# Optimization experiments

Hardware: AMD Instinct MI355X
Metric: run time of the kernel (lower is better)

## Reference

```python
import jax, jax.numpy as jnp
import numpy as np

N, E, G = 50000, 800000, 64
IN, HID, H, OUT = 128, 64, 4, 10


def _gat_layer(x, src, dst, W, a_src, a_dst, b):
    # x: [N, Fin]; W: [H*C, Fin]; a_src/a_dst: [H, C]; b: [H*C]
    n = x.shape[0]
    C = a_src.shape[1]
    h = (x @ W.T).reshape(n, H, C)                      # [N, H, C]
    e_src = jnp.einsum('nhc,hc->nh', h, a_src)          # [N, H]
    e_dst = jnp.einsum('nhc,hc->nh', h, a_dst)          # [N, H]
    logits = jax.nn.leaky_relu(e_src[src] + e_dst[dst], 0.2)  # [E', H]
    # segment softmax over destination node
    m = jax.ops.segment_max(logits, dst, num_segments=n)
    ex = jnp.exp(logits - m[dst])
    denom = jax.ops.segment_sum(ex, dst, num_segments=n)
    alpha = ex / (denom[dst] + 1e-16)                   # [E', H]
    msg = h[src] * alpha[:, :, None]                    # [E', H, C]
    out = jax.ops.segment_sum(msg, dst, num_segments=n) # [N, H, C]
    return out.reshape(n, H * C) + b


def setup_inputs() -> dict:
    key = jax.random.key(0)
    ks = jax.random.split(key, 20)
    x = jax.random.normal(ks[0], (N, IN), dtype=jnp.float32)
    edge_index = jax.random.randint(ks[1], (2, E), 0, N, dtype=jnp.int64)
    batch = jnp.sort(jax.random.randint(ks[2], (N,), 0, G, dtype=jnp.int64))

    def glorot(k, shape):
        fan = shape[-1]
        return jax.random.normal(k, shape, dtype=jnp.float32) / jnp.sqrt(jnp.float32(fan))

    ins = [IN, HID * H, HID * H]
    params = {}
    for i, fin in enumerate(ins, start=1):
        params[f'W{i}'] = glorot(ks[3 * i], (H * HID, fin))
        params[f'a_src{i}'] = glorot(ks[3 * i + 1], (H, HID))
        params[f'a_dst{i}'] = glorot(ks[3 * i + 2], (H, HID))
        params[f'b{i}'] = jnp.zeros((H * HID,), dtype=jnp.float32)
    params['Wl'] = glorot(ks[13], (OUT, H * HID))
    params['bl'] = jnp.zeros((OUT,), dtype=jnp.float32)
    return dict(x=x, edge_index=edge_index, batch=batch, **params)


def reference(x, edge_index, batch,
              W1, a_src1, a_dst1, b1,
              W2, a_src2, a_dst2, b2,
              W3, a_src3, a_dst3, b3,
              Wl, bl):
    n = x.shape[0]
    loops = jnp.arange(n, dtype=edge_index.dtype)
    src = jnp.concatenate([edge_index[0], loops])  # add self-loops (PyG default)
    dst = jnp.concatenate([edge_index[1], loops])

    h = jax.nn.elu(_gat_layer(x, src, dst, W1, a_src1, a_dst1, b1))
    h = jax.nn.elu(_gat_layer(h, src, dst, W2, a_src2, a_dst2, b2))
    h = _gat_layer(h, src, dst, W3, a_src3, a_dst3, b3)

    # global mean pool over graphs
    sums = jax.ops.segment_sum(h, batch, num_segments=G)          # [G, H*HID]
    counts = jax.ops.segment_sum(jnp.ones((n,), h.dtype), batch, num_segments=G)
    pooled = sums / jnp.maximum(counts, 1.0)[:, None]
    return pooled @ Wl.T + bl                                      # [G, OUT]
```

## Files before the change

kernel.cpp:

```cpp
#include <hip/hip_runtime.h>
#include <hip/hip_bf16.h>
#include <math.h>

#define NNODES 50000
#define NEDGES 800000
#define NGRAPH 64
#define FIN 128
#define HC 256
#define NHEAD 4
#define NOUT 10
#define ETOT (NEDGES + NNODES)
#define NB196 ((NNODES + 255) / 256)


typedef unsigned short u16;
typedef unsigned char u8;
typedef __attribute__((ext_vector_type(8))) short short8;
typedef __attribute__((ext_vector_type(4))) float f32x4;
typedef __attribute__((ext_vector_type(2))) float f32x2;

__device__ inline u16 f2b(float f) {
    union { float f; unsigned u; } v; v.f = f;
    unsigned r = v.u + 0x7FFF + ((v.u >> 16) & 1);
    return (u16)(r >> 16);
}
__device__ inline float b2f(u16 u) {
    union { unsigned u; float f; } v; v.u = ((unsigned)u) << 16; return v.f;
}

__device__ inline void gload_lds16(const void* g, void* l) {
    __builtin_amdgcn_global_load_lds(
        (const __attribute__((address_space(1))) unsigned*)g,
        (__attribute__((address_space(3))) unsigned*)l, 16, 0, 0);
}


#define CS0 (NNODES * FIN)
#define CS1 (HC * FIN)
#define CS2 (HC * HC)
#define NBCONV (((CS0 + CS1 + 2 * CS2) / 4 + 255) / 256)
#define NBDEG ((ETOT + 255) / 256)

__global__ void prep_kernel(const float* __restrict__ x, const float* __restrict__ W1,
                            const float* __restrict__ W2, const float* __restrict__ W3,
                            u16* __restrict__ xb, u16* __restrict__ w1b,
                            u16* __restrict__ w2b, u16* __restrict__ w3b,
                            const int* __restrict__ ei, int* __restrict__ deg) {
    int b = blockIdx.x;
    if (b < NBCONV) {
        long i = (long)(b * 256 + threadIdx.x) * 4;
        if (i < CS0) {
            float4 v = *(const float4*)(x + i);
            ushort4 o;
            o.x = f2b(v.x); o.y = f2b(v.y); o.z = f2b(v.z); o.w = f2b(v.w);
            *(ushort4*)(xb + i) = o;
        } else if (i < CS0 + CS1) {
            long off = i - CS0;
            float4 v = *(const float4*)(W1 + off);
            ushort4 o;
            o.x = f2b(v.x); o.y = f2b(v.y); o.z = f2b(v.z); o.w = f2b(v.w);
            *(ushort4*)(w1b + off) = o;
        } else if (i < CS0 + CS1 + 2 * CS2) {
            const float* src; u16* dst; long off;
            if (i < CS0 + CS1 + CS2) { src = W2; dst = w2b; off = i - CS0 - CS1; }
            else                     { src = W3; dst = w3b; off = i - CS0 - CS1 - CS2; }
            float4 v = *(const float4*)(src + off);
            int row = (int)(off >> 8), col = (int)(off & 255);
            float vv[4] = {v.x, v.y, v.z, v.w};
            #pragma unroll
            for (int k = 0; k < 4; ++k) {
                int c = col + k;
                int pp = (c & ~63) | ((c & 15) << 2) | ((c >> 4) & 3);
                dst[row * 256 + pp] = f2b(vv[k]);
            }
        }
    } else {
        int e = (b - NBCONV) * 256 + threadIdx.x;
        if (e >= ETOT) return;
        int dstn = (e < NEDGES) ? ei[NEDGES + e] : (e - NEDGES);
        atomicAdd(&deg[dstn], 1);
    }
}


__global__ __launch_bounds__(256) void scan1_kernel(const int* __restrict__ deg,
                                                    int* __restrict__ off,
                                                    int* __restrict__ bsum) {
    int tid = threadIdx.x, lane = tid & 63, wid = tid >> 6;
    int i = blockIdx.x * 256 + tid;
    __shared__ int ws[4];
    int v = (i < NNODES) ? deg[i] : 0;
    int x = v;
    #pragma unroll
    for (int o = 1; o < 64; o <<= 1) {
        int t = __shfl_up(x, o);
        if (lane >= o) x += t;
    }
    if (lane == 63) ws[wid] = x;
    __syncthreads();
    if (tid < 4) {
        int w = ws[tid];
        #pragma unroll
        for (int o = 1; o < 4; o <<= 1) {
            int t = __shfl_up(w, o, 4);
            if ((tid & 3) >= o) w += t;
        }
        ws[tid] = w;
    }
    __syncthreads();
    int wexcl = wid ? ws[wid - 1] : 0;
    if (i <= NNODES) off[i] = x - v + wexcl;
    if (tid == 0) bsum[blockIdx.x] = ws[3];
}

__global__ __launch_bounds__(256) void scan2_kernel(int* __restrict__ bsum,
                                                    const int* __restrict__ batch,
                                                    int* __restrict__ goff) {
    int tid = threadIdx.x, lane = tid & 63, wid = tid >> 6;
    __shared__ int ws[4];
    int v = (tid < NB196) ? bsum[tid] : 0;
    int x = v;
    #pragma unroll
    for (int o = 1; o < 64; o <<= 1) {
        int t = __shfl_up(x, o);
        if (lane >= o) x += t;
    }
    if (lane == 63) ws[wid] = x;
    __syncthreads();
    if (tid < 4) {
        int w = ws[tid];
        #pragma unroll
        for (int o = 1; o < 4; o <<= 1) {
            int t = __shfl_up(w, o, 4);
            if ((tid & 3) >= o) w += t;
        }
        ws[tid] = w;
    }
    __syncthreads();
    int wexcl = wid ? ws[wid - 1] : 0;
    if (tid < NB196) bsum[tid] = x - v + wexcl;
    if (tid <= NGRAPH) {
        int g = tid, lo = 0, hi = NNODES;
        while (lo < hi) {
            int mid = (lo + hi) >> 1;
            if (batch[mid] < g) lo = mid + 1; else hi = mid;
        }
        goff[g] = lo;
    }
}

__global__ void scatter_kernel(const int* __restrict__ ei, const int* __restrict__ off,
                               const int* __restrict__ bsum,
                               int* __restrict__ cur, int* __restrict__ ssrc) {
    int e = blockIdx.x * blockDim.x + threadIdx.x;
    if (e >= ETOT) return;
    int src, dst;
    if (e < NEDGES) { src = ei[e]; dst = ei[NEDGES + e]; }
    else            { src = dst = e - NEDGES; }
    int pos = off[dst] + bsum[dst >> 8] + atomicAdd(&cur[dst], 1);
    ssrc[pos] = src;
}


#define TBM 128
#define TBN 128
#define TBK 32

__global__ __launch_bounds__(256) void gemm_mfma(const u16* __restrict__ A,
                                                 const u16* __restrict__ B,
                                                 u8* __restrict__ C, int K,
                                                 const float* __restrict__ asrc,
                                                 const float* __restrict__ adst,
                                                 float* __restrict__ es,
                                                 float* __restrict__ ed) {
    __shared__ u16 Als[TBM * TBK];
    __shared__ u16 Bls[TBN * TBK];
    int tid = threadIdx.x;
    int wave = tid >> 6, lane = tid & 63;
    int brow = blockIdx.x * TBM, bcol = blockIdx.y * TBN;
    int m_base = (wave >> 1) * 64, n_base = (wave & 1) * 64;
    int r0 = tid >> 2, kc = (tid & 3) * 8;
    int lquad = lane >> 4, l16 = lane & 15;

    f32x4 acc[4][4] = {};

    const u16* ga0 = A + (size_t)(brow + r0) * K + kc;
    const u16* ga1 = A + (size_t)(brow + 64 + r0) * K + kc;
    const u16* gb0 = B + (size_t)(bcol + r0) * K + kc;
    const u16* gb1 = B + (size_t)(bcol + 64 + r0) * K + kc;
    u16* la0 = &Als[r0 * TBK + kc];
    u16* la1 = &Als[(64 + r0) * TBK + kc];
    u16* lb0 = &Bls[r0 * TBK + kc];
    u16* lb1 = &Bls[(64 + r0) * TBK + kc];

    for (int k0 = 0; k0 < K; k0 += TBK) {
        __syncthreads();
        gload_lds16(ga0 + k0, la0);
        gload_lds16(ga1 + k0, la1);
        gload_lds16(gb0 + k0, lb0);
        gload_lds16(gb1 + k0, lb1);
        __syncthreads();
        short8 fa[4], fb[4];
        #pragma unroll
        for (int i = 0; i < 4; ++i) {
            fa[i] = *(const short8*)(&Als[(m_base + i * 16 + l16) * TBK + lquad * 8]);
            fb[i] = *(const short8*)(&Bls[(n_base + i * 16 + l16) * TBK + lquad * 8]);
        }
        #pragma unroll
        for (int i = 0; i < 4; ++i)
            #pragma unroll
            for (int j = 0; j < 4; ++j)
                acc[i][j] = __builtin_amdgcn_mfma_f32_16x16x32_bf16(fa[i], fb[j], acc[i][j], 0, 0, 0);
    }

    #pragma unroll
    for (int i = 0; i < 4; ++i) {
        int rbase = brow + m_base + i * 16 + lquad * 4;
        #pragma unroll
        for (int r = 0; r < 4; ++r) {
            int row = rbase + r;
            if (row < NNODES) {
                int u = 0;
                u = __builtin_amdgcn_cvt_pk_fp8_f32(acc[i][0][r], acc[i][1][r], u, false);
                u = __builtin_amdgcn_cvt_pk_fp8_f32(acc[i][2][r], acc[i][3][r], u, true);
                *(int*)(C + (size_t)row * HC + bcol + n_base + l16 * 4) = u;
            }
        }
    }

    int head = (bcol + n_base) >> 6;
    float asv[4], adv[4];
    #pragma unroll
    for (int j = 0; j < 4; ++j) {
        asv[j] = asrc[head * 64 + j * 16 + l16];
        adv[j] = adst[head * 64 + j * 16 + l16];
    }
    #pragma unroll
    for (int i = 0; i < 4; ++i) {
        #pragma unroll
        for (int r = 0; r < 4; ++r) {
            float ps = 0.f, pd = 0.f;
            #pragma unroll
            for (int j = 0; j < 4; ++j) {
                ps = fmaf(acc[i][j][r], asv[j], ps);
                pd = fmaf(acc[i][j][r], adv[j], pd);
            }
            #pragma unroll
            for (int o = 1; o < 16; o <<= 1) {
                ps += __shfl_xor(ps, o);
                pd += __shfl_xor(pd, o);
            }
            int row = brow + m_base + i * 16 + lquad * 4 + r;
            if (l16 == 0 && row < NNODES) {
                es[row * 4 + head] = ps;
                ed[row * 4 + head] = pd;
            }
        }
    }
}


__global__ __launch_bounds__(256) void aggregate_kernel(const u8* __restrict__ h,
                                                        const int* __restrict__ ssrc,
                                                        const int* __restrict__ off,
                                                        const int* __restrict__ bsum,
                                                        const float* __restrict__ es,
                                                        const float* __restrict__ ed,
                                                        const float* __restrict__ bias,
                                                        u16* __restrict__ out,
                                                        int apply_elu) {
    __shared__ int2 xch[4][4][17];
    const unsigned* h32 = (const unsigned*)h;
    int wid = threadIdx.x >> 6;
    int dst = blockIdx.x * 4 + wid;
    if (dst >= NNODES) return;
    int lane = threadIdx.x & 63;
    int head = lane >> 4;
    int j16 = lane & 15;
    int s = off[dst] + bsum[dst >> 8];
    int e = off[dst + 1] + bsum[(dst + 1) >> 8];
    float edh = ed[dst * 4 + head];
    int2* myslot = &xch[wid][head][0];

    float a0 = 0.f, a1 = 0.f, a2 = 0.f, a3 = 0.f, dpriv = 0.f;

    int base = s;
    for (; base + 16 <= e; base += 16) {
        int mysrc = ssrc[base + j16];
        float l = es[mysrc * 4 + head] + edh;
        l = fmaxf(l, 0.2f * l);
        float myex = __expf(l);
        dpriv += myex;
        myslot[j16] = make_int2(mysrc, __float_as_int(myex));
        #pragma unroll
        for (int j = 0; j < 16; ++j) {
            int2 pr = myslot[j];
            float exj = __int_as_float(pr.y);
            unsigned hv = h32[(unsigned)pr.x * 64 + lane];
            f32x2 lo = __builtin_amdgcn_cvt_pk_f32_fp8(hv, false);
            f32x2 hi = __builtin_amdgcn_cvt_pk_f32_fp8(hv, true);
            a0 += lo.x * exj;
            a1 += lo.y * exj;
            a2 += hi.x * exj;
            a3 += hi.y * exj;
        }
    }
    int cnt = e - base;
    if (cnt > 0) {
        int mysrc = 0; float myex = 0.f;
        if (j16 < cnt) {
            mysrc = ssrc[base + j16];
            float l = es[mysrc * 4 + head] + edh;
            l = fmaxf(l, 0.2f * l);
            myex = __expf(l);
            dpriv += myex;
        }
        myslot[j16] = make_int2(mysrc, __float_as_int(myex));
        for (int j = 0; j < cnt; ++j) {
            int2 pr = myslot[j];
            float exj = __int_as_float(pr.y);
            unsigned hv = h32[(unsigned)pr.x * 64 + lane];
            f32x2 lo = __builtin_amdgcn_cvt_pk_f32_fp8(hv, false);
            f32x2 hi = __builtin_amdgcn_cvt_pk_f32_fp8(hv, true);
            a0 += lo.x * exj;
            a1 += lo.y * exj;
            a2 += hi.x * exj;
            a3 += hi.y * exj;
        }
    }
    #pragma unroll
    for (int o = 1; o < 16; o <<= 1) dpriv += __shfl_xor(dpriv, o);
    float inv = 1.f / (dpriv + 1e-16f);
    int bbase = ((lane >> 4) << 6) | (lane & 15);
    float b0 = bias[bbase], b1 = bias[bbase + 16], b2 = bias[bbase + 32], b3 = bias[bbase + 48];
    float o0 = a0 * inv + b0;
    float o1 = a1 * inv + b1;
    float o2 = a2 * inv + b2;
    float o3 = a3 * inv + b3;
    if (apply_elu) {
        o0 = o0 > 0.f ? o0 : __expf(o0) - 1.f;
        o1 = o1 > 0.f ? o1 : __expf(o1) - 1.f;
        o2 = o2 > 0.f ? o2 : __expf(o2) - 1.f;
        o3 = o3 > 0.f ? o3 : __expf(o3) - 1.f;
    }
    ushort4 ov;
    ov.x = f2b(o0); ov.y = f2b(o1); ov.z = f2b(o2); ov.w = f2b(o3);
    *(ushort4*)(out + (size_t)dst * HC + lane * 4) = ov;
}


__global__ __launch_bounds__(256) void pool_kernel(const u16* __restrict__ hin,
                                                   const int* __restrict__ goff,
                                                   float* __restrict__ pp) {
    int g = blockIdx.x;
    int slice = blockIdx.y;
    int lane = threadIdx.x & 63;
    int wid = threadIdx.x >> 6;
    int s = goff[g], e = goff[g + 1];
    float a0 = 0.f, a1 = 0.f, a2 = 0.f, a3 = 0.f;
    for (int n = s + slice * 4 + wid; n < e; n += 32) {
        ushort4 hv = *(const ushort4*)(hin + (size_t)n * HC + lane * 4);
        a0 += b2f(hv.x); a1 += b2f(hv.y); a2 += b2f(hv.z); a3 += b2f(hv.w);
    }
    __shared__ float4 part[4][64];
    part[wid][lane] = make_float4(a0, a1, a2, a3);
    __syncthreads();
    if (wid == 0) {
        float4 p0 = part[0][lane], p1 = part[1][lane], p2 = part[2][lane], p3 = part[3][lane];
        float4 v = make_float4((p0.x + p1.x) + (p2.x + p3.x),
                               (p0.y + p1.y) + (p2.y + p3.y),
                               (p0.z + p1.z) + (p2.z + p3.z),
                               (p0.w + p1.w) + (p2.w + p3.w));
        *(float4*)(pp + ((size_t)(g * 8 + slice)) * HC + lane * 4) = v;
    }
}


__global__ __launch_bounds__(64) void final_kernel(const float* __restrict__ pp,
                                                   const int* __restrict__ goff,
                                                   const float* __restrict__ Wl,
                                                   const float* __restrict__ bl,
                                                   float* __restrict__ out) {
    int g = blockIdx.x;
    int lane = threadIdx.x;
    float4 pv = make_float4(0.f, 0.f, 0.f, 0.f);
    #pragma unroll
    for (int sl = 0; sl < 8; ++sl) {
        float4 v = *(const float4*)(pp + ((size_t)(g * 8 + sl)) * HC + lane * 4);
        pv.x += v.x; pv.y += v.y; pv.z += v.z; pv.w += v.w;
    }
    float cntf = fmaxf((float)(goff[g + 1] - goff[g]), 1.f);
    float inv = 1.f / cntf;
    pv.x *= inv; pv.y *= inv; pv.z *= inv; pv.w *= inv;
    int wbase = ((lane >> 4) << 6) | (lane & 15);
    float acc[NOUT];
    #pragma unroll
    for (int o = 0; o < NOUT; ++o) {
        const float* w = Wl + o * HC + wbase;
        acc[o] = pv.x * w[0] + pv.y * w[16] + pv.z * w[32] + pv.w * w[48];
    }
    #pragma unroll
    for (int s = 32; s > 0; s >>= 1)
        #pragma unroll
        for (int o = 0; o < NOUT; ++o)
            acc[o] += __shfl_xor(acc[o], s);
    if (lane == 0) {
        #pragma unroll
        for (int o = 0; o < NOUT; ++o)
            out[g * NOUT + o] = acc[o] + bl[o];
    }
}


extern "C" void kernel_launch(void* const* d_in, const int* in_sizes, int n_in,
                              void* d_out, int out_size, void* d_ws, size_t ws_size,
                              hipStream_t stream) {
    (void)in_sizes; (void)n_in; (void)out_size; (void)ws_size;
    const float* x   = (const float*)d_in[0];
    const int*   ei  = (const int*)d_in[1];
    const int*   bat = (const int*)d_in[2];
    const float* W1  = (const float*)d_in[3];
    const float* as1 = (const float*)d_in[4];
    const float* ad1 = (const float*)d_in[5];
    const float* b1  = (const float*)d_in[6];
    const float* W2  = (const float*)d_in[7];
    const float* as2 = (const float*)d_in[8];
    const float* ad2 = (const float*)d_in[9];
    const float* b2  = (const float*)d_in[10];
    const float* W3  = (const float*)d_in[11];
    const float* as3 = (const float*)d_in[12];
    const float* ad3 = (const float*)d_in[13];
    const float* b3  = (const float*)d_in[14];
    const float* Wl  = (const float*)d_in[15];
    const float* bl  = (const float*)d_in[16];
    float* out = (float*)d_out;

    char* ws = (char*)d_ws;
    size_t p = 0;
    auto alloc = [&](size_t bytes) {
        size_t a = p;
        p += (bytes + 255) & ~(size_t)255;
        return a;
    };
    int*   off  = (int*)(ws + alloc((NNODES + 1) * 4));
    int*   deg  = (int*)(ws + alloc((size_t)NNODES * 4));
    int*   cur  = (int*)(ws + alloc((size_t)NNODES * 4));
    int*   ssrc = (int*)(ws + alloc((size_t)ETOT * 4));
    int*   bsum = (int*)(ws + alloc(256 * 4));
    float* es   = (float*)(ws + alloc((size_t)NNODES * NHEAD * 4));
    float* ed   = (float*)(ws + alloc((size_t)NNODES * NHEAD * 4));
    u16*   xb   = (u16*)(ws + alloc((size_t)NNODES * FIN * 2));
    u16*   w1b  = (u16*)(ws + alloc((size_t)HC * FIN * 2));
    u16*   w2b  = (u16*)(ws + alloc((size_t)HC * HC * 2));
    u16*   w3b  = (u16*)(ws + alloc((size_t)HC * HC * 2));
    u8*    Hb   = (u8*)(ws + alloc((size_t)NNODES * HC));
    u16*   Ab   = (u16*)(ws + alloc((size_t)NNODES * HC * 2));
    float* pp   = (float*)(ws + alloc((size_t)NGRAPH * 8 * HC * 4));
    int*   goff = (int*)(ws + alloc((size_t)(NGRAPH + 1) * 4));
    alloc(128 * 1024);

    hipMemsetAsync(deg, 0, (size_t)((char*)ssrc - (char*)deg), stream);

    prep_kernel<<<NBCONV + NBDEG, 256, 0, stream>>>(x, W1, W2, W3, xb, w1b, w2b, w3b, ei, deg);

    scan1_kernel<<<NB196, 256, 0, stream>>>(deg, off, bsum);
    scan2_kernel<<<1, 256, 0, stream>>>(bsum, bat, goff);
    scatter_kernel<<<NBDEG, 256, 0, stream>>>(ei, off, bsum, cur, ssrc);

    dim3 ggrid((NNODES + TBM - 1) / TBM, HC / TBN);
    int nblocks4 = (NNODES + 3) / 4;

    gemm_mfma<<<ggrid, 256, 0, stream>>>(xb, w1b, Hb, FIN, as1, ad1, es, ed);
    aggregate_kernel<<<nblocks4, 256, 0, stream>>>(Hb, ssrc, off, bsum, es, ed, b1, Ab, 1);
    gemm_mfma<<<ggrid, 256, 0, stream>>>(Ab, w2b, Hb, HC, as2, ad2, es, ed);
    aggregate_kernel<<<nblocks4, 256, 0, stream>>>(Hb, ssrc, off, bsum, es, ed, b2, Ab, 1);
    gemm_mfma<<<ggrid, 256, 0, stream>>>(Ab, w3b, Hb, HC, as3, ad3, es, ed);
    aggregate_kernel<<<nblocks4, 256, 0, stream>>>(Hb, ssrc, off, bsum, es, ed, b3, Ab, 0);

    dim3 pgrid(NGRAPH, 8);
    pool_kernel<<<pgrid, 256, 0, stream>>>(Ab, goff, pp);
    final_kernel<<<NGRAPH, 64, 0, stream>>>(pp, goff, Wl, bl, out);
}
```

Measured before the change: 397.7 us.

## Build CSR via two-pass bucketed scatter with LDS-local ordering

Replaces the per-destination global atomic scatter with two passes. The first pass scatters edges into 256-node buckets using one atomic counter per bucket and packs src with the local destination index. The second pass sorts each bucket in shared memory and writes it out coalesced. This aims to cut contended per-node global atomics and random writes, at the cost of an extra temp buffer, an extra kernel launch, and a hard BUCKET_MAX cap that silently truncates oversized buckets. Packing src into 16 bits also breaks for node ids of 65536 or more, but N is 50000 here so it fits.

After: 893.5 us. +124.6%, slower.

```diff
diff --git a/kernel.cpp b/kernel.cpp
--- a/kernel.cpp
+++ b/kernel.cpp
@@ -11,6 +11,7 @@
 #define NOUT 10
 #define ETOT (NEDGES + NNODES)
 #define NB196 ((NNODES + 255) / 256)
+#define BUCKET_MAX 5376
 
 
 typedef unsigned short u16;
@@ -138,7 +139,7 @@
     }
     __syncthreads();
     int wexcl = wid ? ws[wid - 1] : 0;
-    if (tid < NB196) bsum[tid] = x - v + wexcl;
+    if (tid <= NB196) bsum[tid] = x - v + wexcl;
     if (tid <= NGRAPH) {
         int g = tid, lo = 0, hi = NNODES;
         while (lo < hi) {
@@ -149,16 +150,44 @@
     }
 }
 
-__global__ void scatter_kernel(const int* __restrict__ ei, const int* __restrict__ off,
-                               const int* __restrict__ bsum,
-                               int* __restrict__ cur, int* __restrict__ ssrc) {
+
+__global__ void scatter1_kernel(const int* __restrict__ ei, const int* __restrict__ bsum,
+                                int* __restrict__ bcur, unsigned* __restrict__ tmp) {
     int e = blockIdx.x * blockDim.x + threadIdx.x;
     if (e >= ETOT) return;
     int src, dst;
     if (e < NEDGES) { src = ei[e]; dst = ei[NEDGES + e]; }
     else            { src = dst = e - NEDGES; }
-    int pos = off[dst] + bsum[dst >> 8] + atomicAdd(&cur[dst], 1);
-    ssrc[pos] = src;
+    int bucket = dst >> 8;
+    int pos = bsum[bucket] + atomicAdd(&bcur[bucket], 1);
+    tmp[pos] = (unsigned)src | ((unsigned)(dst & 255) << 16);
+}
+
+__global__ __launch_bounds__(256) void scatter2_kernel(const unsigned* __restrict__ tmp,
+                                                       const int* __restrict__ off,
+                                                       const int* __restrict__ bsum,
+                                                       int* __restrict__ ssrc) {
+    __shared__ int cnt[256];
+    __shared__ int ldss[BUCKET_MAX];
+    int b = blockIdx.x;
+    int tid = threadIdx.x;
+    int s = bsum[b], e2 = bsum[b + 1];
+    int total = e2 - s;
+    if (total > BUCKET_MAX) total = BUCKET_MAX;
+    cnt[tid] = 0;
+    __syncthreads();
+    const int* offb = off + b * 256;
+    for (int i = s + tid; i < e2; i += 256) {
+        unsigned pk = tmp[i];
+        int src = (int)(pk & 0xFFFFu);
+        int ld = (int)(pk >> 16);
+        int rank = atomicAdd(&cnt[ld], 1);
+        int idx = offb[ld] + rank;
+        if (idx < BUCKET_MAX) ldss[idx] = src;
+    }
+    __syncthreads();
+    for (int i = tid; i < total; i += 256)
+        ssrc[s + i] = ldss[i];
 }
 
 
@@ -442,21 +471,22 @@
         p += (bytes + 255) & ~(size_t)255;
         return a;
     };
-    int*   off  = (int*)(ws + alloc((NNODES + 1) * 4));
-    int*   deg  = (int*)(ws + alloc((size_t)NNODES * 4));
-    int*   cur  = (int*)(ws + alloc((size_t)NNODES * 4));
-    int*   ssrc = (int*)(ws + alloc((size_t)ETOT * 4));
-    int*   bsum = (int*)(ws + alloc(256 * 4));
-    float* es   = (float*)(ws + alloc((size_t)NNODES * NHEAD * 4));
-    float* ed   = (float*)(ws + alloc((size_t)NNODES * NHEAD * 4));
-    u16*   xb   = (u16*)(ws + alloc((size_t)NNODES * FIN * 2));
-    u16*   w1b  = (u16*)(ws + alloc((size_t)HC * FIN * 2));
-    u16*   w2b  = (u16*)(ws + alloc((size_t)HC * HC * 2));
-    u16*   w3b  = (u16*)(ws + alloc((size_t)HC * HC * 2));
-    u8*    Hb   = (u8*)(ws + alloc((size_t)NNODES * HC));
-    u16*   Ab   = (u16*)(ws + alloc((size_t)NNODES * HC * 2));
-    float* pp   = (float*)(ws + alloc((size_t)NGRAPH * 8 * HC * 4));
-    int*   goff = (int*)(ws + alloc((size_t)(NGRAPH + 1) * 4));
+    int*      off  = (int*)(ws + alloc((NNODES + 1) * 4));
+    int*      deg  = (int*)(ws + alloc((size_t)NNODES * 4));
+    int*      bcur = (int*)(ws + alloc(256 * 4));
+    int*      ssrc = (int*)(ws + alloc((size_t)ETOT * 4));
+    unsigned* tmp  = (unsigned*)(ws + alloc((size_t)ETOT * 4));
+    int*      bsum = (int*)(ws + alloc(256 * 4));
+    float*    es   = (float*)(ws + alloc((size_t)NNODES * NHEAD * 4));
+    float*    ed   = (float*)(ws + alloc((size_t)NNODES * NHEAD * 4));
+    u16*      xb   = (u16*)(ws + alloc((size_t)NNODES * FIN * 2));
+    u16*      w1b  = (u16*)(ws + alloc((size_t)HC * FIN * 2));
+    u16*      w2b  = (u16*)(ws + alloc((size_t)HC * HC * 2));
+    u16*      w3b  = (u16*)(ws + alloc((size_t)HC * HC * 2));
+    u8*       Hb   = (u8*)(ws + alloc((size_t)NNODES * HC));
+    u16*      Ab   = (u16*)(ws + alloc((size_t)NNODES * HC * 2));
+    float*    pp   = (float*)(ws + alloc((size_t)NGRAPH * 8 * HC * 4));
+    int*      goff = (int*)(ws + alloc((size_t)(NGRAPH + 1) * 4));
     alloc(128 * 1024);
 
     hipMemsetAsync(deg, 0, (size_t)((char*)ssrc - (char*)deg), stream);
@@ -465,7 +495,8 @@
 
     scan1_kernel<<<NB196, 256, 0, stream>>>(deg, off, bsum);
     scan2_kernel<<<1, 256, 0, stream>>>(bsum, bat, goff);
-    scatter_kernel<<<NBDEG, 256, 0, stream>>>(ei, off, bsum, cur, ssrc);
+    scatter1_kernel<<<NBDEG, 256, 0, stream>>>(ei, bsum, bcur, tmp);
+    scatter2_kernel<<<NB196, 256, 0, stream>>>(tmp, off, bsum, ssrc);
 
     dim3 ggrid((NNODES + TBM - 1) / TBM, HC / TBN);
     int nblocks4 = (NNODES + 3) / 4;
```
